# Kernel tuning notes

Hardware: AMD Instinct MI355X
Metric: run time of the kernel (lower is better)

Reference implementation:

```python
import jax, jax.numpy as jnp
from jax import lax
import numpy as np

# dims
B, C, H, W = 16, 64, 56, 56      # input images
N, KH = 1024, 3                  # number of centroids, patch size
K, V = 8, 128                    # k-nearest, values_dim
STRIDE, PAD = 1, 1


def setup_inputs() -> dict:
    key = jax.random.key(0)
    ks = jax.random.split(key, 5)
    x = jax.random.normal(ks[0], (B, C, H, W), jnp.float32)
    centroids = jax.random.normal(ks[1], (N, C, KH, KH), jnp.float32)
    # as in NeighborsValuesAssigner.__init__ (non-whitened path):
    kernel = -centroids                                            # (N,C,3,3)
    bias = 0.5 * jnp.sum(centroids.reshape(N, -1) ** 2, axis=1)    # (N,)
    values = jax.random.normal(ks[2], (N, V), jnp.float32)
    # Conv2d(k*V -> V, kernel 1x1), stored flattened as (V, K*V)
    conv_w = jax.random.normal(ks[3], (V, K * V), jnp.float32) / np.sqrt(K * V)
    conv_b = jax.random.normal(ks[4], (V,), jnp.float32) * 0.01
    return {"x": x, "kernel": kernel, "bias": bias, "values": values,
            "conv_w": conv_w, "conv_b": conv_b}


def reference(x, kernel, bias, values, conv_w, conv_b):
    # distances to centroids via conv (up to a constant 0.5*||patch||^2 per location)
    dist = lax.conv_general_dilated(
        x, kernel, window_strides=(STRIDE, STRIDE),
        padding=[(PAD, PAD), (PAD, PAD)],
        dimension_numbers=("NCHW", "OIHW", "NCHW"))
    dist = dist + bias[None, :, None, None]          # (B, N, Ho, Wo)
    # k smallest distances -> indices (torch.topk(..., largest=False))
    neg = -jnp.transpose(dist, (0, 2, 3, 1))         # (B, Ho, Wo, N)
    _, idx = lax.top_k(neg, K)                       # (B, Ho, Wo, K)
    gathered = values[idx]                           # (B, Ho, Wo, K, V)
    # torch: permute to (B,K,V,H,W), flatten K,V -> channels, 1x1 conv.
    # (B,Ho,Wo,K,V) reshape keeps the same K-outer/V-inner channel order.
    feat = gathered.reshape(gathered.shape[0], gathered.shape[1],
                            gathered.shape[2], K * V)  # (B, Ho, Wo, K*V)
    out = jnp.einsum("bhwc,oc->bohw", feat, conv_w) + conv_b[None, :, None, None]
    return out  # (B, V, Ho, Wo)
```

## Files before the change

### kernel.cpp

```cpp
#include <hip/hip_runtime.h>

#define BATCH   16
#define CH      64
#define NCENT   1024
#define KTOT    576
#define MTOT    50176
#define VDIM    128
#define TOPK    8
#define NSUB    4
#define SK      10
#define POOL    16

typedef float f4 __attribute__((ext_vector_type(4)));
typedef short bf16x8 __attribute__((ext_vector_type(8)));
typedef int i4 __attribute__((ext_vector_type(4)));

__device__ __forceinline__ unsigned short f2bf(float f) {
    union { float f; unsigned u; } c; c.f = f;
    return (unsigned short)((c.u + 0x7fffu + ((c.u >> 16) & 1u)) >> 16);
}
__device__ __forceinline__ unsigned ordkey(float f) {
    unsigned u = __float_as_uint(f);
    return u ^ ((u >> 31) ? 0xFFFFFFFFu : 0x80000000u);
}

__global__ __launch_bounds__(256) void k_prep(const float* __restrict__ kern,
                                              float* __restrict__ kr,
                                              unsigned short* __restrict__ kb) {
    const int o = blockIdx.x * 256 + threadIdx.x;
    const int n = o / 576;
    const int r = o - n * 576;
    const int tap = r >> 6;
    const int c = r & 63;
    const float v = kern[n * 576 + c * 9 + tap];
    kr[o] = v;
    kb[o] = f2bf(v);
}

__global__ __launch_bounds__(256) void k_table(const float* __restrict__ values,
                                               const float* __restrict__ conv_w,
                                               float* __restrict__ table) {
    __shared__ float wk[128][132];
    __shared__ float vals[16][128];

    const int t = threadIdx.x;
    const int k = blockIdx.x >> 6;
    const int n0 = (blockIdx.x & 63) * 16;

    {
        const int row = t >> 1;
        const int seg = (t & 1) * 64;
        const f4* src = (const f4*)(conv_w + row * 1024 + k * 128 + seg);
#pragma unroll
        for (int q = 0; q < 16; ++q) *(f4*)&wk[row][seg + q * 4] = src[q];
    }
    {
        const int r = t >> 4;
        const int col = (t & 15) * 8;
        const f4* src = (const f4*)(values + (n0 + r) * VDIM + col);
        *(f4*)&vals[r][col] = src[0];
        *(f4*)&vals[r][col + 4] = src[1];
    }
    __syncthreads();

    const int o = t & 127;
    const int ngrp = t >> 7;
    float acc[8];
#pragma unroll
    for (int r = 0; r < 8; ++r) acc[r] = 0.f;
    for (int v = 0; v < 128; ++v) {
        const float w = wk[o][v];
#pragma unroll
        for (int r = 0; r < 8; ++r) acc[r] = fmaf(w, vals[ngrp * 8 + r][v], acc[r]);
    }
#pragma unroll
    for (int r = 0; r < 8; ++r) {
        const int n = n0 + ngrp * 8 + r;
        table[(((k << 10) + n) << 7) + o] = acc[r];
    }
}

__global__ __launch_bounds__(256, 3) void k_mfma_topk(const float* __restrict__ x,
                                                      const unsigned short* __restrict__ kb,
                                                      const float* __restrict__ bias,
                                                      unsigned* __restrict__ kws) {
    __shared__ char smem[51200];
    unsigned short* A0 = (unsigned short*)smem;
    unsigned short* A1 = (unsigned short*)(smem + 5120);
    unsigned short* B0 = (unsigned short*)(smem + 10240);
    unsigned short* B1 = (unsigned short*)(smem + 30720);
    float (*dist)[65] = (float (*)[65])(smem + 10240);

    const int t = threadIdx.x;
    const int w = t >> 6;
    const int lane = t & 63;
    const int mfrag = lane & 15;
    const int kq = lane >> 4;

    const int m0 = blockIdx.x * 64;
    const int ml = t & 63;
    const int cg = t >> 6;
    const int L = m0 + ml;
    const int b = L / 3136;
    const int hw = L - b * 3136;
    const int hh = hw / 56;
    const int wp = hw - hh * 56;
    const float* xb = x + b * (CH * 3136);
    const int brow = t >> 2;
    const int bseg = t & 3;

    float top_d[SK];
    unsigned top_k[SK];
#pragma unroll
    for (int j = 0; j < SK; ++j) { top_d[j] = 3.0e38f; top_k[j] = 0xFFFFFFFFu; }

    for (int nt = 0; nt < 4; ++nt) {
        const int n0 = nt * 256;

        f4 acc[4][4];
#pragma unroll
        for (int mi = 0; mi < 4; ++mi)
#pragma unroll
            for (int ni = 0; ni < 4; ++ni) acc[mi][ni] = (f4)0.f;

        {
            const int tap = 0, c0 = 0;
            const int hy = hh + tap / 3 - 1;
            const int wx = wp + tap % 3 - 1;
            const bool inb = ((unsigned)hy < 56u && (unsigned)wx < 56u);
            const float* xp = xb + (c0 + cg * 8) * 3136 + hy * 56 + wx;
            unsigned short tmp[8];
#pragma unroll
            for (int j = 0; j < 8; ++j) tmp[j] = inb ? f2bf(xp[j * 3136]) : (unsigned short)0;
            *(i4*)&A0[ml * 40 + cg * 8] = *(i4*)tmp;
#pragma unroll
            for (int p = 0; p < 4; ++p) {
                const int nn = p * 64 + brow;
                const i4 v = *(const i4*)(kb + (n0 + nn) * KTOT + 0 * 32 + bseg * 8);
                *(i4*)&B0[nn * 40 + bseg * 8] = v;
            }
        }
        __syncthreads();

#pragma unroll 1
        for (int ch = 0; ch < 18; ++ch) {
            unsigned short* Ac = (ch & 1) ? A1 : A0;
            unsigned short* Bc = (ch & 1) ? B1 : B0;
            if (ch < 17) {
                const int chn = ch + 1;
                unsigned short* An = (chn & 1) ? A1 : A0;
                unsigned short* Bn = (chn & 1) ? B1 : B0;
                const int tap = chn >> 1;
                const int c0 = (chn & 1) * 32;
                const int dh = tap / 3;
                const int dw = tap - dh * 3;
                const int hy = hh + dh - 1;
                const int wx = wp + dw - 1;
                const bool inb = ((unsigned)hy < 56u && (unsigned)wx < 56u);
                const float* xp = xb + (c0 + cg * 8) * 3136 + hy * 56 + wx;
                unsigned short tmp[8];
#pragma unroll
                for (int j = 0; j < 8; ++j) tmp[j] = inb ? f2bf(xp[j * 3136]) : (unsigned short)0;
                *(i4*)&An[ml * 40 + cg * 8] = *(i4*)tmp;
#pragma unroll
                for (int p = 0; p < 4; ++p) {
                    const int nn = p * 64 + brow;
                    const i4 v = *(const i4*)(kb + (n0 + nn) * KTOT + chn * 32 + bseg * 8);
                    *(i4*)&Bn[nn * 40 + bseg * 8] = v;
                }
            }
            bf16x8 af[4], bfr[4];
#pragma unroll
            for (int mi = 0; mi < 4; ++mi)
                af[mi] = *(const bf16x8*)&Ac[(mi * 16 + mfrag) * 40 + kq * 8];
#pragma unroll
            for (int ni = 0; ni < 4; ++ni)
                bfr[ni] = *(const bf16x8*)&Bc[(w * 64 + ni * 16 + mfrag) * 40 + kq * 8];
#pragma unroll
            for (int mi = 0; mi < 4; ++mi)
#pragma unroll
                for (int ni = 0; ni < 4; ++ni)
                    acc[mi][ni] = __builtin_amdgcn_mfma_f32_16x16x32_bf16(
                        af[mi], bfr[ni], acc[mi][ni], 0, 0, 0);
            __syncthreads();
        }

        float bv[4];
#pragma unroll
        for (int ni = 0; ni < 4; ++ni)
            bv[ni] = bias[n0 + w * 64 + ni * 16 + mfrag];

#pragma unroll 1
        for (int q = 0; q < 4; ++q) {
            if (w == q) {
#pragma unroll
                for (int mi = 0; mi < 4; ++mi)
#pragma unroll
                    for (int ni = 0; ni < 4; ++ni)
#pragma unroll
                        for (int r = 0; r < 4; ++r)
                            dist[mi * 16 + kq * 4 + r][ni * 16 + mfrag] = acc[mi][ni][r] + bv[ni];
                const int nb = (n0 + q * 64);
                float tlast = top_d[SK - 1];
#pragma unroll 8
                for (int c = 0; c < 64; ++c) {
                    const float v = dist[lane][c];
                    if (v < tlast) {
                        const unsigned key = (ordkey(v) & 0xFFFFFC00u) | (unsigned)(nb + c);
                        top_d[SK - 1] = v; top_k[SK - 1] = key;
#pragma unroll
                        for (int j = SK - 1; j >= 1; --j) {
                            if (top_d[j] < top_d[j - 1]) {
                                const float a = top_d[j]; top_d[j] = top_d[j - 1]; top_d[j - 1] = a;
                                const unsigned kk = top_k[j]; top_k[j] = top_k[j - 1]; top_k[j - 1] = kk;
                            }
                        }
                        tlast = top_d[SK - 1];
                    }
                }
            }
            __syncthreads();
        }
    }

#pragma unroll
    for (int j = 0; j < SK; ++j)
        kws[(w * SK + j) * MTOT + m0 + lane] = top_k[j];
}

__global__ __launch_bounds__(256) void k_refine_out(const float* __restrict__ x,
                                                    const float* __restrict__ kr,
                                                    const float* __restrict__ bias,
                                                    const unsigned* __restrict__ kws,
                                                    const float* __restrict__ table,
                                                    const float* __restrict__ conv_b,
                                                    float* __restrict__ out) {
    __shared__ int   ids[16][POOL];
    __shared__ float dd[16][POOL];
    __shared__ int   id8s[16][TOPK];

    const int t = threadIdx.x;
    const int l0 = blockIdx.x * 16;
    const int b = l0 / 3136;
    const float* xb = x + b * (CH * 3136);

    if (t < 16) {
        const int gl = l0 + t;
        unsigned tk[POOL];
#pragma unroll
        for (int r = 0; r < POOL; ++r) tk[r] = 0xFFFFFFFFu;
#pragma unroll
        for (int s = 0; s < NSUB; ++s)
#pragma unroll
            for (int j = 0; j < SK; ++j) {
                const unsigned k = kws[(s * SK + j) * MTOT + gl];
                if (k < tk[POOL - 1]) {
                    tk[POOL - 1] = k;
#pragma unroll
                    for (int r = POOL - 1; r >= 1; --r) {
                        if (tk[r] < tk[r - 1]) { const unsigned a = tk[r]; tk[r] = tk[r - 1]; tk[r - 1] = a; }
                    }
                }
            }
#pragma unroll
        for (int r = 0; r < POOL; ++r) ids[t][r] = (int)(tk[r] & 1023u);
    }
    __syncthreads();

    {
        const int loc = t & 15;
        const int cand = t >> 4;
        const int gl = l0 + loc;
        const int hw = gl - b * 3136;
        const int hh = hw / 56;
        const int wp = hw - hh * 56;
        const int cd = ids[loc][cand];
        const float* kp = kr + cd * KTOT;
        float a = 0.f;
#pragma unroll 1
        for (int tap = 0; tap < 9; ++tap) {
            const int dh = tap / 3;
            const int dw = tap - dh * 3;
            const int hy = hh + dh - 1;
            const int wx = wp + dw - 1;
            if ((unsigned)hy < 56u && (unsigned)wx < 56u) {
                const float* xp = xb + hy * 56 + wx;
                const float* kt = kp + tap * 64;
#pragma unroll 8
                for (int c = 0; c < 64; ++c)
                    a = fmaf(xp[c * 3136], kt[c], a);
            }
        }
        dd[loc][cand] = a + bias[cd];
    }
    __syncthreads();

    if (t < 16) {
        float td[TOPK]; int ti[TOPK];
#pragma unroll
        for (int j = 0; j < TOPK; ++j) { td[j] = 3.0e38f; ti[j] = 0x7fffffff; }
#pragma unroll
        for (int j = 0; j < POOL; ++j) {
            const float v = dd[t][j];
            const int ii = ids[t][j];
            if (v < td[TOPK - 1] || (v == td[TOPK - 1] && ii < ti[TOPK - 1])) {
                td[TOPK - 1] = v; ti[TOPK - 1] = ii;
#pragma unroll
                for (int q = TOPK - 1; q >= 1; --q) {
                    if (td[q] < td[q - 1] || (td[q] == td[q - 1] && ti[q] < ti[q - 1])) {
                        const float a = td[q]; td[q] = td[q - 1]; td[q - 1] = a;
                        const int bq = ti[q]; ti[q] = ti[q - 1]; ti[q - 1] = bq;
                    }
                }
            }
        }
#pragma unroll
        for (int j = 0; j < TOPK; ++j) id8s[t][j] = ti[j];
    }
    __syncthreads();

    {
        const int loc = t & 15;
        const int og = t >> 4;
        const int gl = l0 + loc;
        const int hw = gl - b * 3136;
        const int o0 = og * 8;
        int idx[TOPK];
#pragma unroll
        for (int j = 0; j < TOPK; ++j) idx[j] = id8s[loc][j];
        f4 a0 = *(const f4*)&conv_b[o0];
        f4 a1 = *(const f4*)&conv_b[o0 + 4];
#pragma unroll
        for (int k = 0; k < TOPK; ++k) {
            const float* row = table + (((k << 10) + idx[k]) << 7) + o0;
            a0 += *(const f4*)&row[0];
            a1 += *(const f4*)&row[4];
        }
        float* ob = out + b * (VDIM * 3136) + hw;
#pragma unroll
        for (int e = 0; e < 4; ++e) {
            ob[(o0 + e) * 3136] = a0[e];
            ob[(o0 + 4 + e) * 3136] = a1[e];
        }
    }
}

extern "C" void kernel_launch(void* const* d_in, const int* in_sizes, int n_in,
                              void* d_out, int out_size, void* d_ws, size_t ws_size,
                              hipStream_t stream) {
    const float* x      = (const float*)d_in[0];
    const float* kern   = (const float*)d_in[1];
    const float* bias   = (const float*)d_in[2];
    const float* values = (const float*)d_in[3];
    const float* conv_w = (const float*)d_in[4];
    const float* conv_b = (const float*)d_in[5];
    float* out = (float*)d_out;

    float* kr = (float*)d_ws;
    unsigned short* kb = (unsigned short*)(kr + NCENT * KTOT);
    float* table = (float*)(kb + NCENT * KTOT);
    unsigned* kws = (unsigned*)(table + 8 * NCENT * VDIM);

    k_prep<<<dim3(NCENT * KTOT / 256), dim3(256), 0, stream>>>(kern, kr, kb);
    k_table<<<dim3(8 * 64), dim3(256), 0, stream>>>(values, conv_w, table);
    k_mfma_topk<<<dim3(MTOT / 64), dim3(256), 0, stream>>>(x, kb, bias, kws);
    k_refine_out<<<dim3(MTOT / 16), dim3(256), 0, stream>>>(x, kr, bias, kws, table, conv_b, out);
}
```

Measured before the change: 989.0 us.

## Fuse MFMA top-k selection with candidate refinement and output gather in one kernel

Merges the MFMA distance/top-k kernel and the refine/output kernel into a single kernel. Per-location candidate keys stay in shared memory instead of going through a global workspace. The per-tile top-k scan now has all four waves scan in parallel over a 64x256 distance tile, replacing the serialized wave-by-wave loop. The fp32 refinement stages input patches through LDS with each thread scoring 4 candidates. In exchange, shared memory per block grows, the occupancy hint drops from 3 to 2 blocks, and extra barriers are added.

```diff
diff --git a/kernel.cpp b/kernel.cpp
--- a/kernel.cpp
+++ b/kernel.cpp
@@ -7,7 +7,6 @@
 #define MTOT    50176
 #define VDIM    128
 #define TOPK    8
-#define NSUB    4
 #define SK      10
 #define POOL    16
 
@@ -80,16 +79,24 @@
     }
 }
 
-__global__ __launch_bounds__(256, 3) void k_mfma_topk(const float* __restrict__ x,
-                                                      const unsigned short* __restrict__ kb,
-                                                      const float* __restrict__ bias,
-                                                      unsigned* __restrict__ kws) {
-    __shared__ char smem[51200];
+__global__ __launch_bounds__(256, 2) void k_fused(const float* __restrict__ x,
+                                                  const unsigned short* __restrict__ kb,
+                                                  const float* __restrict__ kr,
+                                                  const float* __restrict__ bias,
+                                                  const float* __restrict__ table,
+                                                  const float* __restrict__ conv_b,
+                                                  float* __restrict__ out) {
+    __shared__ char smem[65792];
     unsigned short* A0 = (unsigned short*)smem;
     unsigned short* A1 = (unsigned short*)(smem + 5120);
     unsigned short* B0 = (unsigned short*)(smem + 10240);
     unsigned short* B1 = (unsigned short*)(smem + 30720);
-    float (*dist)[65] = (float (*)[65])(smem + 10240);
+    float (*dist)[257] = (float (*)[257])smem;
+    unsigned* keys = (unsigned*)smem;
+    int*      ids  = (int*)(smem + 10496);
+    float*    dd   = (float*)(smem + 14592);
+    int*      id8  = (int*)(smem + 18688);
+    float*    xl   = (float*)(smem + 20736);
 
     const int t = threadIdx.x;
     const int w = t >> 6;
@@ -123,12 +130,13 @@
 #pragma unroll
             for (int ni = 0; ni < 4; ++ni) acc[mi][ni] = (f4)0.f;
 
+        __syncthreads();
+
         {
-            const int tap = 0, c0 = 0;
-            const int hy = hh + tap / 3 - 1;
-            const int wx = wp + tap % 3 - 1;
+            const int hy = hh - 1;
+            const int wx = wp - 1;
             const bool inb = ((unsigned)hy < 56u && (unsigned)wx < 56u);
-            const float* xp = xb + (c0 + cg * 8) * 3136 + hy * 56 + wx;
+            const float* xp = xb + (cg * 8) * 3136 + hy * 56 + wx;
             unsigned short tmp[8];
 #pragma unroll
             for (int j = 0; j < 8; ++j) tmp[j] = inb ? f2bf(xp[j * 3136]) : (unsigned short)0;
@@ -136,7 +144,7 @@
 #pragma unroll
             for (int p = 0; p < 4; ++p) {
                 const int nn = p * 64 + brow;
-                const i4 v = *(const i4*)(kb + (n0 + nn) * KTOT + 0 * 32 + bseg * 8);
+                const i4 v = *(const i4*)(kb + (n0 + nn) * KTOT + bseg * 8);
                 *(i4*)&B0[nn * 40 + bseg * 8] = v;
             }
         }
@@ -185,75 +193,58 @@
             __syncthreads();
         }
 
-        float bv[4];
-#pragma unroll
-        for (int ni = 0; ni < 4; ++ni)
-            bv[ni] = bias[n0 + w * 64 + ni * 16 + mfrag];
-
-#pragma unroll 1
-        for (int q = 0; q < 4; ++q) {
-            if (w == q) {
-#pragma unroll
-                for (int mi = 0; mi < 4; ++mi)
-#pragma unroll
-                    for (int ni = 0; ni < 4; ++ni)
-#pragma unroll
-                        for (int r = 0; r < 4; ++r)
-                            dist[mi * 16 + kq * 4 + r][ni * 16 + mfrag] = acc[mi][ni][r] + bv[ni];
-                const int nb = (n0 + q * 64);
-                float tlast = top_d[SK - 1];
+        {
+            float bv[4];
+#pragma unroll
+            for (int ni = 0; ni < 4; ++ni)
+                bv[ni] = bias[n0 + w * 64 + ni * 16 + mfrag];
+#pragma unroll
+            for (int mi = 0; mi < 4; ++mi)
+#pragma unroll
+                for (int ni = 0; ni < 4; ++ni)
+#pragma unroll
+                    for (int r = 0; r < 4; ++r)
+                        dist[mi * 16 + kq * 4 + r][w * 64 + ni * 16 + mfrag] =
+                            acc[mi][ni][r] + bv[ni];
+        }
+        __syncthreads();
+
+        {
+            const int nb = n0 + cg * 64;
+            float tlast = top_d[SK - 1];
 #pragma unroll 8
-                for (int c = 0; c < 64; ++c) {
-                    const float v = dist[lane][c];
-                    if (v < tlast) {
-                        const unsigned key = (ordkey(v) & 0xFFFFFC00u) | (unsigned)(nb + c);
-                        top_d[SK - 1] = v; top_k[SK - 1] = key;
-#pragma unroll
-                        for (int j = SK - 1; j >= 1; --j) {
-                            if (top_d[j] < top_d[j - 1]) {
-                                const float a = top_d[j]; top_d[j] = top_d[j - 1]; top_d[j - 1] = a;
-                                const unsigned kk = top_k[j]; top_k[j] = top_k[j - 1]; top_k[j - 1] = kk;
-                            }
+            for (int c = 0; c < 64; ++c) {
+                const float v = dist[ml][cg * 64 + c];
+                if (v < tlast) {
+                    const unsigned key = (ordkey(v) & 0xFFFFFC00u) | (unsigned)(nb + c);
+                    top_d[SK - 1] = v; top_k[SK - 1] = key;
+#pragma unroll
+                    for (int j = SK - 1; j >= 1; --j) {
+                        if (top_d[j] < top_d[j - 1]) {
+                            const float a = top_d[j]; top_d[j] = top_d[j - 1]; top_d[j - 1] = a;
+                            const unsigned kk = top_k[j]; top_k[j] = top_k[j - 1]; top_k[j - 1] = kk;
                         }
-                        tlast = top_d[SK - 1];
                     }
+                    tlast = top_d[SK - 1];
                 }
             }
-            __syncthreads();
-        }
-    }
-
-#pragma unroll
-    for (int j = 0; j < SK; ++j)
-        kws[(w * SK + j) * MTOT + m0 + lane] = top_k[j];
-}
-
-__global__ __launch_bounds__(256) void k_refine_out(const float* __restrict__ x,
-                                                    const float* __restrict__ kr,
-                                                    const float* __restrict__ bias,
-                                                    const unsigned* __restrict__ kws,
-                                                    const float* __restrict__ table,
-                                                    const float* __restrict__ conv_b,
-                                                    float* __restrict__ out) {
-    __shared__ int   ids[16][POOL];
-    __shared__ float dd[16][POOL];
-    __shared__ int   id8s[16][TOPK];
-
-    const int t = threadIdx.x;
-    const int l0 = blockIdx.x * 16;
-    const int b = l0 / 3136;
-    const float* xb = x + b * (CH * 3136);
-
-    if (t < 16) {
-        const int gl = l0 + t;
+        }
+    }
+    __syncthreads();
+
+#pragma unroll
+    for (int j = 0; j < SK; ++j) keys[ml * 41 + cg * SK + j] = top_k[j];
+    __syncthreads();
+
+    if (t < 64) {
         unsigned tk[POOL];
 #pragma unroll
         for (int r = 0; r < POOL; ++r) tk[r] = 0xFFFFFFFFu;
 #pragma unroll
-        for (int s = 0; s < NSUB; ++s)
+        for (int s = 0; s < 4; ++s)
 #pragma unroll
             for (int j = 0; j < SK; ++j) {
-                const unsigned k = kws[(s * SK + j) * MTOT + gl];
+                const unsigned k = keys[t * 41 + s * SK + j];
                 if (k < tk[POOL - 1]) {
                     tk[POOL - 1] = k;
 #pragma unroll
@@ -263,46 +254,65 @@
                 }
             }
 #pragma unroll
-        for (int r = 0; r < POOL; ++r) ids[t][r] = (int)(tk[r] & 1023u);
-    }
-    __syncthreads();
-
-    {
-        const int loc = t & 15;
-        const int cand = t >> 4;
-        const int gl = l0 + loc;
-        const int hw = gl - b * 3136;
-        const int hh = hw / 56;
-        const int wp = hw - hh * 56;
-        const int cd = ids[loc][cand];
-        const float* kp = kr + cd * KTOT;
-        float a = 0.f;
+        for (int r = 0; r < POOL; ++r) ids[t * POOL + r] = (int)(tk[r] & 1023u);
+    }
+    __syncthreads();
+
+    int cd[4];
+    const float* kp[4];
+#pragma unroll
+    for (int j = 0; j < 4; ++j) {
+        cd[j] = ids[ml * POOL + cg * 4 + j];
+        kp[j] = kr + cd[j] * KTOT;
+    }
+    float a0 = 0.f, a1 = 0.f, a2 = 0.f, a3 = 0.f;
+
 #pragma unroll 1
-        for (int tap = 0; tap < 9; ++tap) {
-            const int dh = tap / 3;
-            const int dw = tap - dh * 3;
-            const int hy = hh + dh - 1;
-            const int wx = wp + dw - 1;
-            if ((unsigned)hy < 56u && (unsigned)wx < 56u) {
-                const float* xp = xb + hy * 56 + wx;
-                const float* kt = kp + tap * 64;
-#pragma unroll 8
-                for (int c = 0; c < 64; ++c)
-                    a = fmaf(xp[c * 3136], kt[c], a);
-            }
-        }
-        dd[loc][cand] = a + bias[cd];
-    }
-    __syncthreads();
-
-    if (t < 16) {
+    for (int tap = 0; tap < 9; ++tap) {
+        const int dh = tap / 3;
+        const int dw = tap - dh * 3;
+        const int hy = hh + dh - 1;
+        const int wx = wp + dw - 1;
+        const bool inb = ((unsigned)hy < 56u && (unsigned)wx < 56u);
+        __syncthreads();
+#pragma unroll
+        for (int i = 0; i < 16; ++i) {
+            float v = 0.f;
+            if (inb) v = xb[(cg * 16 + i) * 3136 + hy * 56 + wx];
+            xl[ml * 69 + cg * 16 + i] = v;
+        }
+        __syncthreads();
+        const int tb = tap * 64;
+#pragma unroll 4
+        for (int c4 = 0; c4 < 16; ++c4) {
+            const f4 k0 = *(const f4*)&kp[0][tb + c4 * 4];
+            const f4 k1 = *(const f4*)&kp[1][tb + c4 * 4];
+            const f4 k2 = *(const f4*)&kp[2][tb + c4 * 4];
+            const f4 k3 = *(const f4*)&kp[3][tb + c4 * 4];
+#pragma unroll
+            for (int e = 0; e < 4; ++e) {
+                const float xv = xl[ml * 69 + c4 * 4 + e];
+                a0 = fmaf(xv, k0[e], a0);
+                a1 = fmaf(xv, k1[e], a1);
+                a2 = fmaf(xv, k2[e], a2);
+                a3 = fmaf(xv, k3[e], a3);
+            }
+        }
+    }
+    dd[ml * POOL + cg * 4 + 0] = a0 + bias[cd[0]];
+    dd[ml * POOL + cg * 4 + 1] = a1 + bias[cd[1]];
+    dd[ml * POOL + cg * 4 + 2] = a2 + bias[cd[2]];
+    dd[ml * POOL + cg * 4 + 3] = a3 + bias[cd[3]];
+    __syncthreads();
+
+    if (t < 64) {
         float td[TOPK]; int ti[TOPK];
 #pragma unroll
         for (int j = 0; j < TOPK; ++j) { td[j] = 3.0e38f; ti[j] = 0x7fffffff; }
 #pragma unroll
         for (int j = 0; j < POOL; ++j) {
-            const float v = dd[t][j];
-            const int ii = ids[t][j];
+            const float v = dd[t * POOL + j];
+            const int ii = ids[t * POOL + j];
             if (v < td[TOPK - 1] || (v == td[TOPK - 1] && ii < ti[TOPK - 1])) {
                 td[TOPK - 1] = v; ti[TOPK - 1] = ii;
 #pragma unroll
@@ -315,33 +325,30 @@
             }
         }
 #pragma unroll
-        for (int j = 0; j < TOPK; ++j) id8s[t][j] = ti[j];
+        for (int j = 0; j < TOPK; ++j) id8[t * TOPK + j] = ti[j];
     }
     __syncthreads();
 
     {
-        const int loc = t & 15;
-        const int og = t >> 4;
-        const int gl = l0 + loc;
-        const int hw = gl - b * 3136;
-        const int o0 = og * 8;
+        const int o0 = cg * 32;
         int idx[TOPK];
 #pragma unroll
-        for (int j = 0; j < TOPK; ++j) idx[j] = id8s[loc][j];
-        f4 a0 = *(const f4*)&conv_b[o0];
-        f4 a1 = *(const f4*)&conv_b[o0 + 4];
+        for (int j = 0; j < TOPK; ++j) idx[j] = id8[ml * TOPK + j];
+        f4 acc8[8];
+#pragma unroll
+        for (int q = 0; q < 8; ++q) acc8[q] = *(const f4*)&conv_b[o0 + q * 4];
 #pragma unroll
         for (int k = 0; k < TOPK; ++k) {
             const float* row = table + (((k << 10) + idx[k]) << 7) + o0;
-            a0 += *(const f4*)&row[0];
-            a1 += *(const f4*)&row[4];
+#pragma unroll
+            for (int q = 0; q < 8; ++q) acc8[q] += *(const f4*)&row[q * 4];
         }
         float* ob = out + b * (VDIM * 3136) + hw;
 #pragma unroll
-        for (int e = 0; e < 4; ++e) {
-            ob[(o0 + e) * 3136] = a0[e];
-            ob[(o0 + 4 + e) * 3136] = a1[e];
-        }
+        for (int q = 0; q < 8; ++q)
+#pragma unroll
+            for (int e = 0; e < 4; ++e)
+                ob[(o0 + q * 4 + e) * 3136] = acc8[q][e];
     }
 }
 
@@ -359,10 +366,8 @@
     float* kr = (float*)d_ws;
     unsigned short* kb = (unsigned short*)(kr + NCENT * KTOT);
     float* table = (float*)(kb + NCENT * KTOT);
-    unsigned* kws = (unsigned*)(table + 8 * NCENT * VDIM);
 
     k_prep<<<dim3(NCENT * KTOT / 256), dim3(256), 0, stream>>>(kern, kr, kb);
     k_table<<<dim3(8 * 64), dim3(256), 0, stream>>>(values, conv_w, table);
-    k_mfma_topk<<<dim3(MTOT / 64), dim3(256), 0, stream>>>(x, kb, bias, kws);
-    k_refine_out<<<dim3(MTOT / 16), dim3(256), 0, stream>>>(x, kr, bias, kws, table, conv_b, out);
-}
+    k_fused<<<dim3(MTOT / 64), dim3(256), 0, stream>>>(x, kb, kr, bias, table, conv_b, out);
+}
```

After: 871.2 us. -11.9%, faster.
